# Performance work log

Measured on AMD Instinct MI355X. Metric: run time of the kernel, lower is better.

The kernel has to match this reference:

```python
import jax, jax.numpy as jnp
import numpy as np

N = 131072
IN, HID, OUT = 128, 256, 64
NUM_TASKS = 16
NUM_COPIES = 4
NUM_LAYERS = 3


def setup_inputs() -> dict:
    key = jax.random.key(0)
    ks = jax.random.split(key, 10)
    inputs = jax.random.normal(ks[0], (N, IN), dtype=jnp.float32)
    task_indices = jax.random.randint(ks[1], (N,), 0, NUM_TASKS, dtype=jnp.int32)
    copy_maps = jax.random.randint(ks[2], (NUM_LAYERS, NUM_TASKS), 0, NUM_COPIES, dtype=jnp.int32)
    # per-copy Linear weights, Kaiming-ish scale 1/sqrt(fan_in)
    W0 = jax.random.normal(ks[3], (NUM_COPIES, IN, HID), dtype=jnp.float32) / np.sqrt(IN)
    b0 = jax.random.normal(ks[4], (NUM_COPIES, HID), dtype=jnp.float32) * 0.01
    W1 = jax.random.normal(ks[5], (NUM_COPIES, HID, HID), dtype=jnp.float32) / np.sqrt(HID)
    b1 = jax.random.normal(ks[6], (NUM_COPIES, HID), dtype=jnp.float32) * 0.01
    W2 = jax.random.normal(ks[7], (NUM_COPIES, HID, OUT), dtype=jnp.float32) / np.sqrt(HID)
    b2 = jax.random.normal(ks[8], (NUM_COPIES, OUT), dtype=jnp.float32) * 0.01
    return {"inputs": inputs, "task_indices": task_indices, "copy_maps": copy_maps,
            "W0": W0, "b0": b0, "W1": W1, "b1": b1, "W2": W2, "b2": b2}


def _routed_layer(x, W, b, copy_idx, apply_tanh):
    # x: [N, d_in], W: [C, d_in, d_out], b: [C, d_out], copy_idx: [N]
    # Each token goes through exactly one copy's Linear. Equivalent to the
    # torch sort->per-copy-forward->unsort, expressed as masked accumulation
    # over the small fixed set of copies (avoids data-dependent shapes).
    y = jnp.zeros((x.shape[0], W.shape[2]), dtype=x.dtype)
    for c in range(W.shape[0]):
        mask = (copy_idx == c).astype(x.dtype)[:, None]  # [N, 1]
        y = y + mask * (x @ W[c] + b[c])
    return jnp.tanh(y) if apply_tanh else y


def reference(inputs, task_indices, copy_maps, W0, b0, W1, b1, W2, b2):
    x = inputs
    Ws = (W0, W1, W2)
    bs = (b0, b1, b2)
    for layer in range(NUM_LAYERS):
        copy_idx = copy_maps[layer][task_indices]  # [N] task->copy routing
        x = _routed_layer(x, Ws[layer], bs[layer], copy_idx,
                          apply_tanh=(layer != NUM_LAYERS - 1))
    return x
```

## Files before the change

kernel.cpp:

```cpp
#include <hip/hip_runtime.h>

#define N_TOK 131072
#define TILE 32
#define NT_MAX 4112

typedef __attribute__((ext_vector_type(8))) short s8v;
typedef __attribute__((ext_vector_type(4))) float f4v;
typedef unsigned short ushort_t;

__device__ __forceinline__ unsigned short f2bf(float x) {
    union { float f; unsigned u; } v; v.f = x;
    unsigned r = v.u + 0x7fffu + ((v.u >> 16) & 1u);
    return (unsigned short)(r >> 16);
}

__device__ __forceinline__ unsigned pk2(float a, float b) {
    union { float f; unsigned u; } x, y; x.f = a; y.f = b;
    return ((x.u + 0x8000u) >> 16) | ((y.u + 0x8000u) & 0xffff0000u);
}

__device__ __forceinline__ float tanh_fast(float x) {
    float e = __expf(2.0f * x);
    return 1.0f - 2.0f / (e + 1.0f);
}

__global__ void prep_hist_kernel(const float* __restrict__ W0, const float* __restrict__ W1,
                                 const float* __restrict__ W2,
                                 ushort_t* __restrict__ W0p, ushort_t* __restrict__ W1p,
                                 ushort_t* __restrict__ W2p,
                                 const int* __restrict__ task, int* __restrict__ blockCounts) {
    if (blockIdx.x < 224) {
        int f = blockIdx.x * 256 + threadIdx.x;
        const float* src; ushort_t* dst; int K, N;
        if (f < 16384)      { src = W0; dst = W0p; K = 128; N = 256; }
        else if (f < 49152) { src = W1; dst = W1p; K = 256; N = 256; f -= 16384; }
        else                { src = W2; dst = W2p; K = 256; N = 64;  f -= 49152; }
        int fpc = (N >> 4) * (K >> 5) * 64;
        int c = f / fpc, r = f % fpc;
        int lane = r & 63;
        int kt = (r >> 6) % (K >> 5);
        int ftile = (r >> 6) / (K >> 5);
        int n = ftile * 16 + (lane & 15);
        int kbase = kt * 32 + (lane >> 4) * 8;
        const float* s = src + (size_t)c * K * N + (size_t)kbase * N + n;
        s8v pk;
#pragma unroll
        for (int j = 0; j < 8; j++) pk[j] = (short)f2bf(s[(size_t)j * N]);
        *reinterpret_cast<s8v*>(dst + ((size_t)(c * fpc + r) << 3)) = pk;
    } else {
        __shared__ int cnt[16];
        int t = threadIdx.x;
        int hb = blockIdx.x - 224;
        if (t < 16) cnt[t] = 0;
        __syncthreads();
        int base = hb * 2048 + t;
#pragma unroll
        for (int i = 0; i < 8; i++) atomicAdd(&cnt[task[base + i * 256]], 1);
        __syncthreads();
        if (t < 16) blockCounts[hb * 16 + t] = cnt[t];
    }
}

__global__ void sort_kernel(const int* __restrict__ task, const int* __restrict__ blockCounts,
                            int* __restrict__ tileTask, int* __restrict__ nT,
                            int* __restrict__ perm) {
    __shared__ int cntLds[1024];
    __shared__ int total[16], pref[16], rank[16];
    __shared__ int tokBase[16], tbase[17];
    int t = threadIdx.x, b = blockIdx.x;
    for (int i = t; i < 1024; i += 256) cntLds[i] = blockCounts[i];
    if (t < 16) rank[t] = 0;
    __syncthreads();
    if (t < 16) {
        int tot = 0, pf = 0;
#pragma unroll
        for (int bb = 0; bb < 64; bb++) {
            int v = cntLds[bb * 16 + t];
            tot += v;
            if (bb < b) pf += v;
        }
        total[t] = tot; pref[t] = pf;
    }
    __syncthreads();
    if (t == 0) {
        int tok = 0, tile = 0;
        for (int k = 0; k < 16; k++) {
            tokBase[k] = tok;
            tbase[k] = tile;
            int ntk = (total[k] + TILE - 1) / TILE;
            tok += ntk * TILE;
            tile += ntk;
        }
        tbase[16] = tile;
        if (b == 0) nT[0] = tile;
    }
    __syncthreads();
    if (b == 0) {
        for (int i = t; i < NT_MAX; i += 256) {
            int tk = 0;
            if (i < tbase[16]) {
#pragma unroll
                for (int k = 0; k < 16; k++) if (i >= tbase[k]) tk = k;
            }
            tileTask[i] = tk;
        }
    }
    int tk[8], my[8];
#pragma unroll
    for (int i = 0; i < 8; i++) {
        int idx = b * 2048 + i * 256 + t;
        tk[i] = task[idx];
        my[i] = atomicAdd(&rank[tk[i]], 1);
    }
#pragma unroll
    for (int i = 0; i < 8; i++) {
        int idx = b * 2048 + i * 256 + t;
        perm[tokBase[tk[i]] + pref[tk[i]] + my[i]] = idx;
    }
}

__launch_bounds__(512, 8)
__global__ void mlp_kernel(const float* __restrict__ x_in,
                           const int* __restrict__ cmap,
                           const float* __restrict__ b0,
                           const float* __restrict__ b1,
                           const float* __restrict__ b2,
                           const ushort_t* __restrict__ W0p,
                           const ushort_t* __restrict__ W1p,
                           const ushort_t* __restrict__ W2p,
                           const int* __restrict__ tileTask,
                           const int* __restrict__ nTp,
                           const int* __restrict__ perm,
                           float* __restrict__ out) {
    __shared__ __align__(16) ushort_t H1[8192];
    __shared__ __align__(16) ushort_t XH2[8192];
    __shared__ int toks[TILE];

    int b = blockIdx.x;
    if (b >= nTp[0]) return;
    int t = threadIdx.x;
    int task = tileTask[b];
    int c0 = cmap[task], c1 = cmap[16 + task], c2 = cmap[32 + task];

    int w = t >> 6;
    int lane = t & 63;
    int l15 = lane & 15, lq = lane >> 4;

    {
        int r = t >> 4, q = t & 15;
        int tok = perm[b * TILE + r];
        if (q == 0) toks[r] = tok;
        float4 v0 = make_float4(0.f, 0.f, 0.f, 0.f), v1 = v0;
        if ((unsigned)tok < (unsigned)N_TOK) {
            const float4* src = reinterpret_cast<const float4*>(x_in) + (size_t)tok * 32 + q * 2;
            v0 = src[0]; v1 = src[1];
        }
        int fragid = (r >> 4) * 4 + (q >> 2);
        int lanep = (r & 15) + 16 * (q & 3);
        uint4 pk;
        pk.x = pk2(v0.x, v0.y); pk.y = pk2(v0.z, v0.w);
        pk.z = pk2(v1.x, v1.y); pk.w = pk2(v1.z, v1.w);
        *reinterpret_cast<uint4*>(&XH2[(fragid * 64 + lanep) << 3]) = pk;
    }
    __syncthreads();

    {
        f4v acc[2][2];
#pragma unroll
        for (int mi = 0; mi < 2; mi++)
#pragma unroll
            for (int nt = 0; nt < 2; nt++) { f4v z = {0.f, 0.f, 0.f, 0.f}; acc[mi][nt] = z; }
        const ushort_t* Wc = W0p + (size_t)c0 * 32768;
#pragma unroll
        for (int kt = 0; kt < 4; kt++) {
            s8v wa[2];
#pragma unroll
            for (int mi = 0; mi < 2; mi++)
                wa[mi] = *reinterpret_cast<const s8v*>(Wc + ((((2 * w + mi) * 4 + kt) * 64 + lane) << 3));
            s8v xb[2];
#pragma unroll
            for (int nt = 0; nt < 2; nt++)
                xb[nt] = *reinterpret_cast<const s8v*>(&XH2[((nt * 4 + kt) * 64 + lane) << 3]);
#pragma unroll
            for (int mi = 0; mi < 2; mi++)
#pragma unroll
                for (int nt = 0; nt < 2; nt++)
                    acc[mi][nt] = __builtin_amdgcn_mfma_f32_16x16x32_bf16(wa[mi], xb[nt], acc[mi][nt], 0, 0, 0);
        }
#pragma unroll
        for (int mi = 0; mi < 2; mi++) {
            int ft = 2 * w + mi;
            float4 bv = *reinterpret_cast<const float4*>(b0 + c0 * 256 + ft * 16 + lq * 4);
            int kt_h = ft >> 1;
            int lanep = l15 + 16 * ((ft & 1) * 2 + (lq >> 1));
            int j0 = (lq & 1) * 4;
#pragma unroll
            for (int nt = 0; nt < 2; nt++) {
                float t0 = tanh_fast(acc[mi][nt][0] + bv.x);
                float t1 = tanh_fast(acc[mi][nt][1] + bv.y);
                float t2 = tanh_fast(acc[mi][nt][2] + bv.z);
                float t3 = tanh_fast(acc[mi][nt][3] + bv.w);
                uint2 pk; pk.x = pk2(t0, t1); pk.y = pk2(t2, t3);
                *reinterpret_cast<uint2*>(&H1[(((nt * 8 + kt_h) * 64 + lanep) << 3) + j0]) = pk;
            }
        }
    }
    __syncthreads();

    {
        f4v acc[2][2];
#pragma unroll
        for (int mi = 0; mi < 2; mi++)
#pragma unroll
            for (int nt = 0; nt < 2; nt++) { f4v z = {0.f, 0.f, 0.f, 0.f}; acc[mi][nt] = z; }
        const ushort_t* Wc = W1p + (size_t)c1 * 65536;
#pragma unroll
        for (int kt = 0; kt < 8; kt++) {
            s8v wa[2];
#pragma unroll
            for (int mi = 0; mi < 2; mi++)
                wa[mi] = *reinterpret_cast<const s8v*>(Wc + ((((2 * w + mi) * 8 + kt) * 64 + lane) << 3));
            s8v xb[2];
#pragma unroll
            for (int nt = 0; nt < 2; nt++)
                xb[nt] = *reinterpret_cast<const s8v*>(&H1[((nt * 8 + kt) * 64 + lane) << 3]);
#pragma unroll
            for (int mi = 0; mi < 2; mi++)
#pragma unroll
                for (int nt = 0; nt < 2; nt++)
                    acc[mi][nt] = __builtin_amdgcn_mfma_f32_16x16x32_bf16(wa[mi], xb[nt], acc[mi][nt], 0, 0, 0);
        }
#pragma unroll
        for (int mi = 0; mi < 2; mi++) {
            int ft = 2 * w + mi;
            float4 bv = *reinterpret_cast<const float4*>(b1 + c1 * 256 + ft * 16 + lq * 4);
            int kt_h = ft >> 1;
            int lanep = l15 + 16 * ((ft & 1) * 2 + (lq >> 1));
            int j0 = (lq & 1) * 4;
#pragma unroll
            for (int nt = 0; nt < 2; nt++) {
                float t0 = tanh_fast(acc[mi][nt][0] + bv.x);
                float t1 = tanh_fast(acc[mi][nt][1] + bv.y);
                float t2 = tanh_fast(acc[mi][nt][2] + bv.z);
                float t3 = tanh_fast(acc[mi][nt][3] + bv.w);
                uint2 pk; pk.x = pk2(t0, t1); pk.y = pk2(t2, t3);
                *reinterpret_cast<uint2*>(&XH2[(((nt * 8 + kt_h) * 64 + lanep) << 3) + j0]) = pk;
            }
        }
    }
    __syncthreads();

    {
        int mt = w & 3, nt = w >> 2;
        f4v acc = {0.f, 0.f, 0.f, 0.f};
        const ushort_t* Wc = W2p + (size_t)c2 * 16384;
#pragma unroll
        for (int kt = 0; kt < 8; kt++) {
            s8v wa = *reinterpret_cast<const s8v*>(Wc + (((mt * 8 + kt) * 64 + lane) << 3));
            s8v xb = *reinterpret_cast<const s8v*>(&XH2[((nt * 8 + kt) * 64 + lane) << 3]);
            acc = __builtin_amdgcn_mfma_f32_16x16x32_bf16(wa, xb, acc, 0, 0, 0);
        }
        int tok = toks[nt * 16 + l15];
        if ((unsigned)tok < (unsigned)N_TOK) {
            float4 bv = *reinterpret_cast<const float4*>(b2 + c2 * 64 + mt * 16 + lq * 4);
            float4 o;
            o.x = acc[0] + bv.x; o.y = acc[1] + bv.y;
            o.z = acc[2] + bv.z; o.w = acc[3] + bv.w;
            *reinterpret_cast<float4*>(out + (size_t)tok * 64 + mt * 16 + lq * 4) = o;
        }
    }
}

extern "C" void kernel_launch(void* const* d_in, const int* in_sizes, int n_in,
                              void* d_out, int out_size, void* d_ws, size_t ws_size,
                              hipStream_t stream) {
    const float* inputs = (const float*)d_in[0];
    const int*   task   = (const int*)d_in[1];
    const int*   cmap   = (const int*)d_in[2];
    const float* W0     = (const float*)d_in[3];
    const float* b0     = (const float*)d_in[4];
    const float* W1     = (const float*)d_in[5];
    const float* b1     = (const float*)d_in[6];
    const float* W2     = (const float*)d_in[7];
    const float* b2     = (const float*)d_in[8];
    float* out = (float*)d_out;

    char* ws = (char*)d_ws;
    int* blockCounts = (int*)(ws + 0);
    int* nT          = (int*)(ws + 4096);
    int* tileTask    = (int*)(ws + 4160);
    int* perm        = (int*)(ws + 20608);
    ushort_t* W0p    = (ushort_t*)(ws + 546944);
    ushort_t* W1p    = (ushort_t*)(ws + 809088);
    ushort_t* W2p    = (ushort_t*)(ws + 1333376);

    prep_hist_kernel<<<288, 256, 0, stream>>>(W0, W1, W2, W0p, W1p, W2p, task, blockCounts);
    sort_kernel<<<64, 256, 0, stream>>>(task, blockCounts, tileTask, nT, perm);
    mlp_kernel<<<NT_MAX, 512, 0, stream>>>(inputs, cmap, b0, b1, b2,
                                           W0p, W1p, W2p, tileTask, nT, perm, out);
}
```

Before: 175.3 us.

## Use 128-token tiles with 32x32x16 MFMA and padded row-major LDS activations

Raises the token tile from 32 to 128 so each block reuses the routed weight fragments across four times as many tokens, and switches from 16x16x32 to 32x32x16 bf16 MFMA. Activations are kept in padded row-major LDS buffers, and the prepacked weights' K order is permuted so that the 32x32 MFMA output layout can feed the next layer's B operand directly. Biases are preloaded into the accumulators instead of being added afterwards. The larger LDS footprint and more accumulator registers lower occupancy, and tiles padded per task waste more work.

```diff
diff --git a/kernel.cpp b/kernel.cpp
--- a/kernel.cpp
+++ b/kernel.cpp
@@ -1,11 +1,13 @@
 #include <hip/hip_runtime.h>
 
 #define N_TOK 131072
-#define TILE 32
-#define NT_MAX 4112
+#define TILE 128
+#define NT_MAX 1040
+#define XS 136
+#define HS 264
 
 typedef __attribute__((ext_vector_type(8))) short s8v;
-typedef __attribute__((ext_vector_type(4))) float f4v;
+typedef __attribute__((ext_vector_type(16))) float f16v;
 typedef unsigned short ushort_t;
 
 __device__ __forceinline__ unsigned short f2bf(float x) {
@@ -22,6 +24,11 @@
 __device__ __forceinline__ float tanh_fast(float x) {
     float e = __expf(2.0f * x);
     return 1.0f - 2.0f / (e + 1.0f);
+}
+
+__device__ __forceinline__ int phi(int s) {
+    int lh = s >> 4, rg = s & 15;
+    return (rg & 3) + 8 * (rg >> 2) + 4 * lh;
 }
 
 __global__ void prep_hist_kernel(const float* __restrict__ W0, const float* __restrict__ W1,
@@ -30,23 +37,25 @@
                                  ushort_t* __restrict__ W2p,
                                  const int* __restrict__ task, int* __restrict__ blockCounts) {
     if (blockIdx.x < 224) {
-        int f = blockIdx.x * 256 + threadIdx.x;
-        const float* src; ushort_t* dst; int K, N;
-        if (f < 16384)      { src = W0; dst = W0p; K = 128; N = 256; }
-        else if (f < 49152) { src = W1; dst = W1p; K = 256; N = 256; f -= 16384; }
-        else                { src = W2; dst = W2p; K = 256; N = 64;  f -= 49152; }
-        int fpc = (N >> 4) * (K >> 5) * 64;
-        int c = f / fpc, r = f % fpc;
-        int lane = r & 63;
-        int kt = (r >> 6) % (K >> 5);
-        int ftile = (r >> 6) / (K >> 5);
-        int n = ftile * 16 + (lane & 15);
-        int kbase = kt * 32 + (lane >> 4) * 8;
-        const float* s = src + (size_t)c * K * N + (size_t)kbase * N + n;
+        int i = blockIdx.x * 256 + threadIdx.x;
+        const float* src; ushort_t* dst; int K, N, permk;
+        if (i < 16384)      { src = W0; dst = W0p; K = 128; N = 256; permk = 0; }
+        else if (i < 49152) { src = W1; dst = W1p; K = 256; N = 256; permk = 1; i -= 16384; }
+        else                { src = W2; dst = W2p; K = 256; N = 64;  permk = 1; i -= 49152; }
+        int lane = i & 63, fr = i >> 6;
+        int KT = K >> 4;
+        int fpc = (N >> 5) * KT;
+        int c = fr / fpc, r = fr % fpc;
+        int F = r / KT, kt = r % KT;
+        int fphys = F * 32 + (lane & 31);
         s8v pk;
 #pragma unroll
-        for (int j = 0; j < 8; j++) pk[j] = (short)f2bf(s[(size_t)j * N]);
-        *reinterpret_cast<s8v*>(dst + ((size_t)(c * fpc + r) << 3)) = pk;
+        for (int j = 0; j < 8; j++) {
+            int ks = kt * 16 + ((lane >> 5) << 3) + j;
+            int kp = permk ? ((ks & ~31) + phi(ks & 31)) : ks;
+            pk[j] = (short)f2bf(src[((size_t)c * K + kp) * N + fphys]);
+        }
+        *reinterpret_cast<s8v*>(dst + ((size_t)(fr * 64 + lane) << 3)) = pk;
     } else {
         __shared__ int cnt[16];
         int t = threadIdx.x;
@@ -119,7 +128,7 @@
     }
 }
 
-__launch_bounds__(512, 8)
+__launch_bounds__(512, 2)
 __global__ void mlp_kernel(const float* __restrict__ x_in,
                            const int* __restrict__ cmap,
                            const float* __restrict__ b0,
@@ -132,8 +141,8 @@
                            const int* __restrict__ nTp,
                            const int* __restrict__ perm,
                            float* __restrict__ out) {
-    __shared__ __align__(16) ushort_t H1[8192];
-    __shared__ __align__(16) ushort_t XH2[8192];
+    __shared__ __align__(16) ushort_t H1[TILE * HS];
+    __shared__ __align__(16) ushort_t XH2[TILE * HS];
     __shared__ int toks[TILE];
 
     int b = blockIdx.x;
@@ -142,131 +151,175 @@
     int task = tileTask[b];
     int c0 = cmap[task], c1 = cmap[16 + task], c2 = cmap[32 + task];
 
+    {
+        int r = t >> 2, q = t & 3;
+        int tok = perm[b * TILE + r];
+        if (q == 0) toks[r] = tok;
+        float4 v[8];
+        if ((unsigned)tok < (unsigned)N_TOK) {
+            const float4* src = reinterpret_cast<const float4*>(x_in) + (size_t)tok * 32 + q * 8;
+#pragma unroll
+            for (int i = 0; i < 8; i++) v[i] = src[i];
+        } else {
+#pragma unroll
+            for (int i = 0; i < 8; i++) v[i] = make_float4(0.f, 0.f, 0.f, 0.f);
+        }
+        ushort_t* dst = &XH2[r * XS + q * 32];
+#pragma unroll
+        for (int h = 0; h < 2; h++) {
+            uint4 pk;
+            pk.x = pk2(v[4 * h + 0].x, v[4 * h + 0].y); pk.y = pk2(v[4 * h + 0].z, v[4 * h + 0].w);
+            pk.z = pk2(v[4 * h + 1].x, v[4 * h + 1].y); pk.w = pk2(v[4 * h + 1].z, v[4 * h + 1].w);
+            *reinterpret_cast<uint4*>(dst + h * 16) = pk;
+            uint4 pk_b;
+            pk_b.x = pk2(v[4 * h + 2].x, v[4 * h + 2].y); pk_b.y = pk2(v[4 * h + 2].z, v[4 * h + 2].w);
+            pk_b.z = pk2(v[4 * h + 3].x, v[4 * h + 3].y); pk_b.w = pk2(v[4 * h + 3].z, v[4 * h + 3].w);
+            *reinterpret_cast<uint4*>(dst + h * 16 + 8) = pk_b;
+        }
+    }
+    __syncthreads();
+
     int w = t >> 6;
     int lane = t & 63;
-    int l15 = lane & 15, lq = lane >> 4;
+    int l31 = lane & 31, lh = lane >> 5;
 
     {
-        int r = t >> 4, q = t & 15;
-        int tok = perm[b * TILE + r];
-        if (q == 0) toks[r] = tok;
-        float4 v0 = make_float4(0.f, 0.f, 0.f, 0.f), v1 = v0;
-        if ((unsigned)tok < (unsigned)N_TOK) {
-            const float4* src = reinterpret_cast<const float4*>(x_in) + (size_t)tok * 32 + q * 2;
-            v0 = src[0]; v1 = src[1];
-        }
-        int fragid = (r >> 4) * 4 + (q >> 2);
-        int lanep = (r & 15) + 16 * (q & 3);
-        uint4 pk;
-        pk.x = pk2(v0.x, v0.y); pk.y = pk2(v0.z, v0.w);
-        pk.z = pk2(v1.x, v1.y); pk.w = pk2(v1.z, v1.w);
-        *reinterpret_cast<uint4*>(&XH2[(fragid * 64 + lanep) << 3]) = pk;
-    }
-    __syncthreads();
-
-    {
-        f4v acc[2][2];
-#pragma unroll
-        for (int mi = 0; mi < 2; mi++)
-#pragma unroll
-            for (int nt = 0; nt < 2; nt++) { f4v z = {0.f, 0.f, 0.f, 0.f}; acc[mi][nt] = z; }
+        int p = w & 1, fg = w >> 1;
+        f16v acc[2][2];
+#pragma unroll
+        for (int mi = 0; mi < 2; mi++) {
+            int F = 2 * fg + mi;
+#pragma unroll
+            for (int g = 0; g < 4; g++) {
+                float4 bv = *reinterpret_cast<const float4*>(b0 + c0 * 256 + F * 32 + g * 8 + 4 * lh);
+#pragma unroll
+                for (int nt = 0; nt < 2; nt++) {
+                    acc[mi][nt][g * 4 + 0] = bv.x; acc[mi][nt][g * 4 + 1] = bv.y;
+                    acc[mi][nt][g * 4 + 2] = bv.z; acc[mi][nt][g * 4 + 3] = bv.w;
+                }
+            }
+        }
         const ushort_t* Wc = W0p + (size_t)c0 * 32768;
-#pragma unroll
-        for (int kt = 0; kt < 4; kt++) {
-            s8v wa[2];
-#pragma unroll
-            for (int mi = 0; mi < 2; mi++)
-                wa[mi] = *reinterpret_cast<const s8v*>(Wc + ((((2 * w + mi) * 4 + kt) * 64 + lane) << 3));
-            s8v xb[2];
-#pragma unroll
-            for (int nt = 0; nt < 2; nt++)
-                xb[nt] = *reinterpret_cast<const s8v*>(&XH2[((nt * 4 + kt) * 64 + lane) << 3]);
-#pragma unroll
-            for (int mi = 0; mi < 2; mi++)
-#pragma unroll
-                for (int nt = 0; nt < 2; nt++)
-                    acc[mi][nt] = __builtin_amdgcn_mfma_f32_16x16x32_bf16(wa[mi], xb[nt], acc[mi][nt], 0, 0, 0);
-        }
-#pragma unroll
-        for (int mi = 0; mi < 2; mi++) {
-            int ft = 2 * w + mi;
-            float4 bv = *reinterpret_cast<const float4*>(b0 + c0 * 256 + ft * 16 + lq * 4);
-            int kt_h = ft >> 1;
-            int lanep = l15 + 16 * ((ft & 1) * 2 + (lq >> 1));
-            int j0 = (lq & 1) * 4;
-#pragma unroll
-            for (int nt = 0; nt < 2; nt++) {
-                float t0 = tanh_fast(acc[mi][nt][0] + bv.x);
-                float t1 = tanh_fast(acc[mi][nt][1] + bv.y);
-                float t2 = tanh_fast(acc[mi][nt][2] + bv.z);
-                float t3 = tanh_fast(acc[mi][nt][3] + bv.w);
-                uint2 pk; pk.x = pk2(t0, t1); pk.y = pk2(t2, t3);
-                *reinterpret_cast<uint2*>(&H1[(((nt * 8 + kt_h) * 64 + lanep) << 3) + j0]) = pk;
-            }
-        }
-    }
-    __syncthreads();
-
-    {
-        f4v acc[2][2];
-#pragma unroll
-        for (int mi = 0; mi < 2; mi++)
-#pragma unroll
-            for (int nt = 0; nt < 2; nt++) { f4v z = {0.f, 0.f, 0.f, 0.f}; acc[mi][nt] = z; }
-        const ushort_t* Wc = W1p + (size_t)c1 * 65536;
 #pragma unroll
         for (int kt = 0; kt < 8; kt++) {
             s8v wa[2];
 #pragma unroll
             for (int mi = 0; mi < 2; mi++)
-                wa[mi] = *reinterpret_cast<const s8v*>(Wc + ((((2 * w + mi) * 8 + kt) * 64 + lane) << 3));
+                wa[mi] = *reinterpret_cast<const s8v*>(Wc + ((((2 * fg + mi) * 8 + kt) * 64 + lane) << 3));
             s8v xb[2];
 #pragma unroll
             for (int nt = 0; nt < 2; nt++)
-                xb[nt] = *reinterpret_cast<const s8v*>(&H1[((nt * 8 + kt) * 64 + lane) << 3]);
+                xb[nt] = *reinterpret_cast<const s8v*>(&XH2[((2 * p + nt) * 32 + l31) * XS + kt * 16 + lh * 8]);
 #pragma unroll
             for (int mi = 0; mi < 2; mi++)
 #pragma unroll
                 for (int nt = 0; nt < 2; nt++)
-                    acc[mi][nt] = __builtin_amdgcn_mfma_f32_16x16x32_bf16(wa[mi], xb[nt], acc[mi][nt], 0, 0, 0);
+                    acc[mi][nt] = __builtin_amdgcn_mfma_f32_32x32x16_bf16(wa[mi], xb[nt], acc[mi][nt], 0, 0, 0);
         }
 #pragma unroll
         for (int mi = 0; mi < 2; mi++) {
-            int ft = 2 * w + mi;
-            float4 bv = *reinterpret_cast<const float4*>(b1 + c1 * 256 + ft * 16 + lq * 4);
-            int kt_h = ft >> 1;
-            int lanep = l15 + 16 * ((ft & 1) * 2 + (lq >> 1));
-            int j0 = (lq & 1) * 4;
+            int F = 2 * fg + mi;
 #pragma unroll
             for (int nt = 0; nt < 2; nt++) {
-                float t0 = tanh_fast(acc[mi][nt][0] + bv.x);
-                float t1 = tanh_fast(acc[mi][nt][1] + bv.y);
-                float t2 = tanh_fast(acc[mi][nt][2] + bv.z);
-                float t3 = tanh_fast(acc[mi][nt][3] + bv.w);
-                uint2 pk; pk.x = pk2(t0, t1); pk.y = pk2(t2, t3);
-                *reinterpret_cast<uint2*>(&XH2[(((nt * 8 + kt_h) * 64 + lanep) << 3) + j0]) = pk;
+                ushort_t* dst = &H1[((2 * p + nt) * 32 + l31) * HS + F * 32 + lh * 16];
+                uint4 o;
+                o.x = pk2(tanh_fast(acc[mi][nt][0]), tanh_fast(acc[mi][nt][1]));
+                o.y = pk2(tanh_fast(acc[mi][nt][2]), tanh_fast(acc[mi][nt][3]));
+                o.z = pk2(tanh_fast(acc[mi][nt][4]), tanh_fast(acc[mi][nt][5]));
+                o.w = pk2(tanh_fast(acc[mi][nt][6]), tanh_fast(acc[mi][nt][7]));
+                *reinterpret_cast<uint4*>(dst) = o;
+                uint4 o2;
+                o2.x = pk2(tanh_fast(acc[mi][nt][8]),  tanh_fast(acc[mi][nt][9]));
+                o2.y = pk2(tanh_fast(acc[mi][nt][10]), tanh_fast(acc[mi][nt][11]));
+                o2.z = pk2(tanh_fast(acc[mi][nt][12]), tanh_fast(acc[mi][nt][13]));
+                o2.w = pk2(tanh_fast(acc[mi][nt][14]), tanh_fast(acc[mi][nt][15]));
+                *reinterpret_cast<uint4*>(dst + 8) = o2;
             }
         }
     }
     __syncthreads();
 
     {
-        int mt = w & 3, nt = w >> 2;
-        f4v acc = {0.f, 0.f, 0.f, 0.f};
+        int p = w & 1, fg = w >> 1;
+        f16v acc[2][2];
+#pragma unroll
+        for (int mi = 0; mi < 2; mi++) {
+            int F = 2 * fg + mi;
+#pragma unroll
+            for (int g = 0; g < 4; g++) {
+                float4 bv = *reinterpret_cast<const float4*>(b1 + c1 * 256 + F * 32 + g * 8 + 4 * lh);
+#pragma unroll
+                for (int nt = 0; nt < 2; nt++) {
+                    acc[mi][nt][g * 4 + 0] = bv.x; acc[mi][nt][g * 4 + 1] = bv.y;
+                    acc[mi][nt][g * 4 + 2] = bv.z; acc[mi][nt][g * 4 + 3] = bv.w;
+                }
+            }
+        }
+        const ushort_t* Wc = W1p + (size_t)c1 * 65536;
+#pragma unroll
+        for (int kt = 0; kt < 16; kt++) {
+            s8v wa[2];
+#pragma unroll
+            for (int mi = 0; mi < 2; mi++)
+                wa[mi] = *reinterpret_cast<const s8v*>(Wc + ((((2 * fg + mi) * 16 + kt) * 64 + lane) << 3));
+            s8v xb[2];
+#pragma unroll
+            for (int nt = 0; nt < 2; nt++)
+                xb[nt] = *reinterpret_cast<const s8v*>(&H1[((2 * p + nt) * 32 + l31) * HS + kt * 16 + lh * 8]);
+#pragma unroll
+            for (int mi = 0; mi < 2; mi++)
+#pragma unroll
+                for (int nt = 0; nt < 2; nt++)
+                    acc[mi][nt] = __builtin_amdgcn_mfma_f32_32x32x16_bf16(wa[mi], xb[nt], acc[mi][nt], 0, 0, 0);
+        }
+#pragma unroll
+        for (int mi = 0; mi < 2; mi++) {
+            int F = 2 * fg + mi;
+#pragma unroll
+            for (int nt = 0; nt < 2; nt++) {
+                ushort_t* dst = &XH2[((2 * p + nt) * 32 + l31) * HS + F * 32 + lh * 16];
+                uint4 o;
+                o.x = pk2(tanh_fast(acc[mi][nt][0]), tanh_fast(acc[mi][nt][1]));
+                o.y = pk2(tanh_fast(acc[mi][nt][2]), tanh_fast(acc[mi][nt][3]));
+                o.z = pk2(tanh_fast(acc[mi][nt][4]), tanh_fast(acc[mi][nt][5]));
+                o.w = pk2(tanh_fast(acc[mi][nt][6]), tanh_fast(acc[mi][nt][7]));
+                *reinterpret_cast<uint4*>(dst) = o;
+                uint4 o2;
+                o2.x = pk2(tanh_fast(acc[mi][nt][8]),  tanh_fast(acc[mi][nt][9]));
+                o2.y = pk2(tanh_fast(acc[mi][nt][10]), tanh_fast(acc[mi][nt][11]));
+                o2.z = pk2(tanh_fast(acc[mi][nt][12]), tanh_fast(acc[mi][nt][13]));
+                o2.w = pk2(tanh_fast(acc[mi][nt][14]), tanh_fast(acc[mi][nt][15]));
+                *reinterpret_cast<uint4*>(dst + 8) = o2;
+            }
+        }
+    }
+    __syncthreads();
+
+    {
+        int tt = w & 3, F = w >> 2;
+        f16v acc;
+#pragma unroll
+        for (int g = 0; g < 4; g++) {
+            float4 bv = *reinterpret_cast<const float4*>(b2 + c2 * 64 + F * 32 + g * 8 + 4 * lh);
+            acc[g * 4 + 0] = bv.x; acc[g * 4 + 1] = bv.y;
+            acc[g * 4 + 2] = bv.z; acc[g * 4 + 3] = bv.w;
+        }
         const ushort_t* Wc = W2p + (size_t)c2 * 16384;
 #pragma unroll
-        for (int kt = 0; kt < 8; kt++) {
-            s8v wa = *reinterpret_cast<const s8v*>(Wc + (((mt * 8 + kt) * 64 + lane) << 3));
-            s8v xb = *reinterpret_cast<const s8v*>(&XH2[((nt * 8 + kt) * 64 + lane) << 3]);
-            acc = __builtin_amdgcn_mfma_f32_16x16x32_bf16(wa, xb, acc, 0, 0, 0);
-        }
-        int tok = toks[nt * 16 + l15];
+        for (int kt = 0; kt < 16; kt++) {
+            s8v wa = *reinterpret_cast<const s8v*>(Wc + (((F * 16 + kt) * 64 + lane) << 3));
+            s8v xb = *reinterpret_cast<const s8v*>(&XH2[(tt * 32 + l31) * HS + kt * 16 + lh * 8]);
+            acc = __builtin_amdgcn_mfma_f32_32x32x16_bf16(wa, xb, acc, 0, 0, 0);
+        }
+        int tok = toks[tt * 32 + l31];
         if ((unsigned)tok < (unsigned)N_TOK) {
-            float4 bv = *reinterpret_cast<const float4*>(b2 + c2 * 64 + mt * 16 + lq * 4);
-            float4 o;
-            o.x = acc[0] + bv.x; o.y = acc[1] + bv.y;
-            o.z = acc[2] + bv.z; o.w = acc[3] + bv.w;
-            *reinterpret_cast<float4*>(out + (size_t)tok * 64 + mt * 16 + lq * 4) = o;
+#pragma unroll
+            for (int g = 0; g < 4; g++) {
+                float4 o;
+                o.x = acc[g * 4 + 0]; o.y = acc[g * 4 + 1];
+                o.z = acc[g * 4 + 2]; o.w = acc[g * 4 + 3];
+                *reinterpret_cast<float4*>(out + (size_t)tok * 64 + F * 32 + g * 8 + 4 * lh) = o;
+            }
         }
     }
 }
@@ -289,10 +342,10 @@
     int* blockCounts = (int*)(ws + 0);
     int* nT          = (int*)(ws + 4096);
     int* tileTask    = (int*)(ws + 4160);
-    int* perm        = (int*)(ws + 20608);
-    ushort_t* W0p    = (ushort_t*)(ws + 546944);
-    ushort_t* W1p    = (ushort_t*)(ws + 809088);
-    ushort_t* W2p    = (ushort_t*)(ws + 1333376);
+    int* perm        = (int*)(ws + 8320);
+    ushort_t* W0p    = (ushort_t*)(ws + 540800);
+    ushort_t* W1p    = (ushort_t*)(ws + 802944);
+    ushort_t* W2p    = (ushort_t*)(ws + 1327232);
 
     prep_hist_kernel<<<288, 256, 0, stream>>>(W0, W1, W2, W0p, W1p, W2p, task, blockCounts);
     sort_kernel<<<64, 256, 0, stream>>>(task, blockCounts, tileTask, nT, perm);
```

Measured after the change: 213.0 us. 21.5% more time.
